# Optimization experiments

Measured on AMD Instinct MI355X. Metric: run time of the kernel, lower is better.

Reference implementation:

```python
import jax, jax.numpy as jnp
import numpy as np

B, C, H, W = 2, 64, 256, 256
CQ = C // 8    # query/key channels
CR = C // 16   # ShareChannelAttention reduction


def _conv1x1(x, w, b):
    # x: [B,C,H,W], w: [O,C], b: [O]  (1x1 conv == per-pixel linear)
    return jnp.einsum('bchw,oc->bohw', x, w) + b[None, :, None, None]


def _criss_cross(q, k, v):
    # q,k: [B,CQ,H,W], v: [B,C,H,W]; row+column attention with -inf on the
    # H-diagonal, softmax over concatenated H+W energies.
    Hh = q.shape[2]
    eH = jnp.einsum('bchw,bcgw->bhwg', q, k)                 # column (over h') energies
    eH = jnp.where(jnp.eye(Hh, dtype=bool)[:, None, :], -jnp.inf, eH)
    eW = jnp.einsum('bchw,bchv->bhwv', q, k)                 # row (over w') energies
    att = jax.nn.softmax(jnp.concatenate([eH, eW], axis=-1), axis=-1)  # [B,H,W,H+W]
    aH, aW = att[..., :Hh], att[..., Hh:]
    outH = jnp.einsum('bhwg,bcgw->bchw', aH, v)
    outW = jnp.einsum('bhwv,bchv->bchw', aW, v)
    return outH + outW


def _shareca(xa, xb, w1, b1, w2, b2):
    s = xa + xb
    def mlp(p):
        return _conv1x1(jax.nn.relu(_conv1x1(p, w1, b1)), w2, b2)
    gate = jax.nn.sigmoid(mlp(s.mean(axis=(2, 3), keepdims=True)) +
                          mlp(s.max(axis=(2, 3), keepdims=True)))
    return gate * s  # gate*xa + gate*xb


def _bn_relu(x, scale, bias):
    # BatchNorm2d in training mode (batch statistics, biased variance), eps=1e-5
    m = x.mean(axis=(0, 2, 3), keepdims=True)
    v = x.var(axis=(0, 2, 3), keepdims=True)
    xn = (x - m) * jax.lax.rsqrt(v + 1e-5)
    return jax.nn.relu(xn * scale[None, :, None, None] + bias[None, :, None, None])


def setup_inputs() -> dict:
    key = jax.random.key(0)
    ks = jax.random.split(key, 32)
    def n(k, shape, s=0.05):
        return jax.random.normal(k, shape, dtype=jnp.float32) * s
    inp = {
        'x1': n(ks[0], (B, C, H, W), 1.0),
        'x2': n(ks[1], (B, C, H, W), 1.0),
        'wq1': n(ks[2], (CQ, C)), 'bq1': n(ks[3], (CQ,)),
        'wq2': n(ks[4], (CQ, C)), 'bq2': n(ks[5], (CQ,)),
        'wk1': n(ks[6], (CQ, C)), 'bk1': n(ks[7], (CQ,)),
        'wk2': n(ks[8], (CQ, C)), 'bk2': n(ks[9], (CQ,)),
        'wv1': n(ks[10], (C, C)), 'bv1': n(ks[11], (C,)),
        'wv2': n(ks[12], (C, C)), 'bv2': n(ks[13], (C,)),
        'gamma1': n(ks[14], (1,), 0.5), 'gamma2': n(ks[15], (1,), 0.5),
        'sc1_w1': n(ks[16], (CR, C)), 'sc1_b1': n(ks[17], (CR,)),
        'sc1_w2': n(ks[18], (C, CR)), 'sc1_b2': n(ks[19], (C,)),
        'sc2_w1': n(ks[20], (CR, C)), 'sc2_b1': n(ks[21], (CR,)),
        'sc2_w2': n(ks[22], (C, CR)), 'sc2_b2': n(ks[23], (C,)),
        'bn1_scale': jnp.ones((C,), jnp.float32), 'bn1_bias': n(ks[24], (C,)),
        'bn2_scale': jnp.ones((C,), jnp.float32), 'bn2_bias': n(ks[25], (C,)),
    }
    return inp


def reference(x1, x2, wq1, bq1, wq2, bq2, wk1, bk1, wk2, bk2,
              wv1, bv1, wv2, bv2, gamma1, gamma2,
              sc1_w1, sc1_b1, sc1_w2, sc1_b2,
              sc2_w1, sc2_b1, sc2_w2, sc2_b2,
              bn1_scale, bn1_bias, bn2_scale, bn2_bias):
    q1 = _conv1x1(x1, wq1, bq1); q2 = _conv1x1(x2, wq2, bq2)
    k1 = _conv1x1(x1, wk1, bk1); k2 = _conv1x1(x2, wk2, bk2)
    v1 = _conv1x1(x1, wv1, bv1); v2 = _conv1x1(x2, wv2, bv2)
    att1 = _criss_cross(q2, k1, v1)  # out_H_1 + out_W_1
    att2 = _criss_cross(q1, k2, v2)  # out_H_2 + out_W_2
    x_1 = _shareca(gamma2 * att2 + x2, x1, sc1_w1, sc1_b1, sc1_w2, sc1_b2)
    x_2 = _shareca(gamma1 * att1 + x1, x2, sc2_w1, sc2_b1, sc2_w2, sc2_b2)
    out1 = _bn_relu(x_1 + x1, bn1_scale, bn1_bias)
    out2 = _bn_relu(x_2 + x2, bn2_scale, bn2_bias)
    # channel exchange: even channels keep the original input
    mask = (jnp.arange(C) % 2 == 0)[None, :, None, None]
    return jnp.where(mask, x1, out1), jnp.where(mask, x2, out2)
```

## Files before the change

kernel.cpp:

```cpp
#include <hip/hip_runtime.h>
#include <hip/hip_bf16.h>
#include <cstdint>
#include <cstddef>

typedef unsigned short bf16t;
typedef __attribute__((ext_vector_type(8))) short bf16x8;
typedef __attribute__((ext_vector_type(4))) float f32x4;

__device__ __forceinline__ unsigned short f2bf(float f) {
    unsigned u = __float_as_uint(f);
    u += 0x7fffu + ((u >> 16) & 1u);
    return (unsigned short)(u >> 16);
}
__device__ __forceinline__ float bf2f(unsigned short h) {
    return __uint_as_float(((unsigned)h) << 16);
}
__device__ __forceinline__ float bflo(unsigned u) { return __uint_as_float(u << 16); }
__device__ __forceinline__ float bfhi(unsigned u) { return __uint_as_float(u & 0xffff0000u); }
__device__ __forceinline__ unsigned pk2(float a, float b) {
    __hip_bfloat162 h = __float22bfloat162_rn(make_float2(a, b));
    return *(unsigned*)&h;
}
__device__ __forceinline__ bf16x8 mk8(unsigned a, unsigned b, unsigned c, unsigned d) {
    union { uint4 u; bf16x8 v; } cv; cv.u = make_uint4(a, b, c, d); return cv.v;
}

__device__ __forceinline__ unsigned fenc(float f) {
    unsigned u = __float_as_uint(f);
    return (u & 0x80000000u) ? ~u : (u | 0x80000000u);
}
__device__ __forceinline__ float fdec(unsigned u) {
    return __uint_as_float((u & 0x80000000u) ? (u ^ 0x80000000u) : ~u);
}

#define HW 65536

struct ConvArgs {
    const float* x[2];
    const float* wq[2]; const float* bq[2];
    const float* wk[2]; const float* bk[2];
    const float* wv[2]; const float* bv[2];
    bf16t* q[2]; bf16t* k[2]; bf16t* v[2];
    unsigned* zeroR;
};

__global__ __launch_bounds__(256) void conv_qkv(ConvArgs A)
{
    __shared__ __align__(16) bf16t Xlds[256 * 68];

    const int t = threadIdx.x;
    const int z = blockIdx.z;
    const int s = z >> 1, b = z & 1;
    if (z == 0 && blockIdx.x == 0) {
#pragma unroll
        for (int i = 0; i < 6; i++) A.zeroR[t + i * 256] = 0u;
    }
    const int lane = t & 63, wv = t >> 6, quad = lane >> 4, l16 = lane & 15;
    const int px0 = blockIdx.x * 256;

    const float* xp = A.x[s] + (size_t)b * 64 * HW + px0 + t;
    {
        unsigned xw[32];
#pragma unroll
        for (int c = 0; c < 32; c++)
            xw[c] = pk2(xp[(size_t)(2 * c) * HW], xp[(size_t)(2 * c + 1) * HW]);
#pragma unroll
        for (int g = 0; g < 16; g++)
            *(uint2*)&Xlds[t * 68 + g * 4] = make_uint2(xw[2 * g], xw[2 * g + 1]);
    }

    bf16x8 bfr[5][2];
    float bo[5];
    bf16t* obase[5];
#pragma unroll
    for (int ot = 0; ot < 5; ot++) {
        const int o = ot * 16 + l16;
        const float* wrow;
        if (o < 8)       { wrow = A.wq[s] + o * 64;        bo[ot] = A.bq[s][o];
                           obase[ot] = A.q[s] + (size_t)(b * 8 + o) * HW; }
        else if (o < 16) { wrow = A.wk[s] + (o - 8) * 64;  bo[ot] = A.bk[s][o - 8];
                           obase[ot] = A.k[s] + (size_t)(b * 8 + o - 8) * HW; }
        else             { wrow = A.wv[s] + (o - 16) * 64; bo[ot] = A.bv[s][o - 16];
                           obase[ot] = A.v[s] + (size_t)(b * 64 + o - 16) * HW; }
#pragma unroll
        for (int ks = 0; ks < 2; ks++) {
            const float* wp = wrow + ks * 32 + quad * 8;
            bfr[ot][ks] = mk8(pk2(wp[0], wp[1]), pk2(wp[2], wp[3]),
                              pk2(wp[4], wp[5]), pk2(wp[6], wp[7]));
        }
    }

    __syncthreads();

    bf16x8 afr[4][2];
#pragma unroll
    for (int i = 0; i < 4; i++)
#pragma unroll
        for (int ks = 0; ks < 2; ks++) {
            const int base = (wv * 64 + i * 16 + l16) * 68 + ks * 32 + quad * 8;
            const uint2 lo = *(const uint2*)&Xlds[base];
            const uint2 hi = *(const uint2*)&Xlds[base + 4];
            afr[i][ks] = mk8(lo.x, lo.y, hi.x, hi.y);
        }

    const f32x4 z4 = {0.f, 0.f, 0.f, 0.f};
    f32x4 acc[4][5];
#pragma unroll
    for (int i = 0; i < 4; i++)
#pragma unroll
        for (int ot = 0; ot < 5; ot++) acc[i][ot] = z4;

#pragma unroll
    for (int ks = 0; ks < 2; ks++)
#pragma unroll
        for (int i = 0; i < 4; i++)
#pragma unroll
            for (int ot = 0; ot < 5; ot++)
                acc[i][ot] = __builtin_amdgcn_mfma_f32_16x16x32_bf16(afr[i][ks], bfr[ot][ks], acc[i][ot], 0, 0, 0);

#pragma unroll
    for (int i = 0; i < 4; i++) {
        const int px = px0 + wv * 64 + i * 16 + quad * 4;
#pragma unroll
        for (int ot = 0; ot < 5; ot++) {
            uint2 u;
            u.x = pk2(acc[i][ot][0] + bo[ot], acc[i][ot][1] + bo[ot]);
            u.y = pk2(acc[i][ot][2] + bo[ot], acc[i][ot][3] + bo[ot]);
            *(uint2*)&obase[ot][px] = u;
        }
    }
}

__global__ __launch_bounds__(256) void transpose16(const bf16t* __restrict__ in, bf16t* __restrict__ out)
{
    __shared__ bf16t tile[64][68];
    const size_t zo = (size_t)blockIdx.z * HW;
    const int i0 = blockIdx.y * 64, j0 = blockIdx.x * 64;
    const int lc = threadIdx.x & 63, rg = threadIdx.x >> 6;
#pragma unroll
    for (int rr = 0; rr < 16; rr++) {
        int row = rg * 16 + rr;
        tile[row][lc] = in[zo + (size_t)(i0 + row) * 256 + j0 + lc];
    }
    __syncthreads();
#pragma unroll
    for (int rr = 0; rr < 16; rr++) {
        int row = rg * 16 + rr;
        out[zo + (size_t)(j0 + row) * 256 + i0 + lc] = tile[lc][row];
    }
}

struct RowccArgs {
    const bf16t* q[4]; const bf16t* k[4]; const bf16t* v[4];
    bf16t* o[4]; float* so[4];
};

__global__ __launch_bounds__(256, 3) void rowcc_mfma(RowccArgs P)
{
    __shared__ __align__(16) bf16t vs[64 * 264];

    const int t = threadIdx.x;
    const int r = blockIdx.x, b = blockIdx.y, z = blockIdx.z;
    const bool mask = (z < 2);
    const int lane = t & 63, wv = t >> 6, quad = lane >> 4, l16 = lane & 15;
    const int wband = wv * 64;
    const int jperm = 8 * (l16 >> 2) + (l16 & 3);

    const bf16t* qp = P.q[z];
    const bf16t* kp = P.k[z];
    const bf16t* vp = P.v[z];

    const size_t vb = (size_t)b * 64 * HW + (size_t)r * 256;
#pragma unroll
    for (int i = 0; i < 8; i++) {
        const int qd = i * 256 + t;
        const int c = qd >> 5, jc = (qd & 31) * 8;
        *(uint4*)&vs[c * 264 + jc] = *(const uint4*)&vp[vb + (size_t)c * HW + jc];
    }

    const bf16x8 zfr = {0, 0, 0, 0, 0, 0, 0, 0};
    bf16x8 qfr[4] = {zfr, zfr, zfr, zfr};
    const size_t rowb = (size_t)b * 8 * HW + (size_t)r * 256;
    if (quad == 0) {
#pragma unroll
        for (int wt = 0; wt < 4; wt++) {
            const int w_g = wband + wt * 16 + l16;
#pragma unroll
            for (int ch = 0; ch < 8; ch++)
                qfr[wt][ch] = (short)qp[rowb + (size_t)ch * HW + w_g];
        }
    }

    const f32x4 z4 = {0.f, 0.f, 0.f, 0.f};
    f32x4 acc[4][4];
#pragma unroll
    for (int i = 0; i < 4; i++)
#pragma unroll
        for (int j = 0; j < 4; j++) acc[i][j] = z4;
    float s_t[4] = {0.f, 0.f, 0.f, 0.f};

    bf16x8 kcur[2] = {zfr, zfr};
    if (quad == 0) {
#pragma unroll
        for (int jtile = 0; jtile < 2; jtile++)
#pragma unroll
            for (int ch = 0; ch < 8; ch++)
                kcur[jtile][ch] = (short)kp[rowb + (size_t)ch * HW + jtile * 4 + jperm];
    }

    __syncthreads();

    for (int jt = 0; jt < 8; jt++) {
        const int j0 = jt * 32;

        bf16x8 bfr[4];
#pragma unroll
        for (int ct = 0; ct < 4; ct++)
            bfr[ct] = *(const bf16x8*)&vs[(ct * 16 + l16) * 264 + j0 + quad * 8];

        bf16x8 knext[2] = {zfr, zfr};
        if (jt < 7 && quad == 0) {
            const int jn = (jt + 1) * 32;
#pragma unroll
            for (int jtile = 0; jtile < 2; jtile++)
#pragma unroll
                for (int ch = 0; ch < 8; ch++)
                    knext[jtile][ch] = (short)kp[rowb + (size_t)ch * HW + jn + jtile * 4 + jperm];
        }

        const bool dodiag = mask && ((jt >> 1) == wv);

#pragma unroll
        for (int wt = 0; wt < 4; wt++) {
            f32x4 e0 = __builtin_amdgcn_mfma_f32_16x16x32_bf16(kcur[0], qfr[wt], z4, 0, 0, 0);
            f32x4 e1 = __builtin_amdgcn_mfma_f32_16x16x32_bf16(kcur[1], qfr[wt], z4, 0, 0, 0);

            if (dodiag) {
                const int w_g = wband + wt * 16 + l16;
                const int jb = j0 + 8 * quad;
#pragma unroll
                for (int rr = 0; rr < 4; rr++) {
                    if (jb + rr == w_g)     e0[rr] = -3.0e38f;
                    if (jb + 4 + rr == w_g) e1[rr] = -3.0e38f;
                }
            }

            float p[8];
#pragma unroll
            for (int rr = 0; rr < 4; rr++) {
                p[rr]     = __expf(e0[rr]);
                p[4 + rr] = __expf(e1[rr]);
            }
            s_t[wt] += ((p[0] + p[1]) + (p[2] + p[3])) + ((p[4] + p[5]) + (p[6] + p[7]));
            const bf16x8 pa = mk8(pk2(p[0], p[1]), pk2(p[2], p[3]),
                                  pk2(p[4], p[5]), pk2(p[6], p[7]));

#pragma unroll
            for (int ct = 0; ct < 4; ct++)
                acc[wt][ct] = __builtin_amdgcn_mfma_f32_16x16x32_bf16(pa, bfr[ct], acc[wt][ct], 0, 0, 0);
        }

        kcur[0] = knext[0]; kcur[1] = knext[1];
    }

#pragma unroll
    for (int wt = 0; wt < 4; wt++) {
        float s = s_t[wt];
        s += __shfl_xor(s, 16, 64);
        s += __shfl_xor(s, 32, 64);
        s_t[wt] = s;
    }
    if (quad == 0) {
#pragma unroll
        for (int wt = 0; wt < 4; wt++) {
            const int w_g = wband + wt * 16 + l16;
            if (mask)
                P.so[z][(size_t)b * HW + w_g * 256 + r] = s_t[wt];
            else
                P.so[z][(size_t)b * HW + r * 256 + w_g] = s_t[wt];
        }
    }

    __syncthreads();
    bf16t* o_lds = vs;
#pragma unroll
    for (int wt = 0; wt < 4; wt++) {
        const int w0 = wband + wt * 16 + quad * 4;
#pragma unroll
        for (int ct = 0; ct < 4; ct++) {
            const int c = ct * 16 + l16;
            uint2 u;
            u.x = pk2(acc[wt][ct][0], acc[wt][ct][1]);
            u.y = pk2(acc[wt][ct][2], acc[wt][ct][3]);
            *(uint2*)&o_lds[c * 264 + w0] = u;
        }
    }
    __syncthreads();
    bf16t* ob = P.o[z] + (size_t)b * 64 * HW + (size_t)r * 256;
#pragma unroll
    for (int i = 0; i < 8; i++) {
        const int qd = i * 256 + t;
        const int c = qd >> 5, w8 = (qd & 31) * 8;
        *(uint4*)&ob[(size_t)c * HW + w8] = *(const uint4*)&o_lds[c * 264 + w8];
    }
}

__global__ __launch_bounds__(256) void combine_reduce(
    const bf16t* __restrict__ oH1, const bf16t* __restrict__ oW1,
    const bf16t* __restrict__ oH2, const bf16t* __restrict__ oW2,
    const float* __restrict__ sH1, const float* __restrict__ sW1,
    const float* __restrict__ sH2, const float* __restrict__ sW2,
    const float* __restrict__ x1, const float* __restrict__ x2,
    const float* __restrict__ gamma1, const float* __restrict__ gamma2,
    bf16t* __restrict__ s1, bf16t* __restrict__ s2,
    float* __restrict__ accum, unsigned* __restrict__ accmax)
{
    const int t = threadIdx.x, chunk = blockIdx.x, c = blockIdx.y, b = blockIdx.z;
    const float g1v = gamma1[0], g2v = gamma2[0];
    const size_t cb = ((size_t)(b * 64 + c)) * HW;
    const size_t pb = (size_t)b * HW;
    const bool codd = (c & 1) != 0;

    float pS1 = 0, pSS1 = 0, pSX1 = 0, pX1 = 0, pXX1 = 0, pM1 = -3e38f;
    float pS2 = 0, pSS2 = 0, pSX2 = 0, pX2 = 0, pXX2 = 0, pM2 = -3e38f;

    for (int i = 0; i < 16; i++) {
        const int pidx = chunk * 4096 + i * 256 + t;
        const float inv1 = 1.f / (sH1[pb + pidx] + sW1[pb + pidx]);
        const float inv2 = 1.f / (sH2[pb + pidx] + sW2[pb + pidx]);
        const float a1 = (bf2f(oH1[cb + pidx]) + bf2f(oW1[cb + pidx])) * inv1;
        const float a2 = (bf2f(oH2[cb + pidx]) + bf2f(oW2[cb + pidx])) * inv2;
        const float x1v = x1[cb + pidx], x2v = x2[cb + pidx];
        const float s1v = g2v * a2 + x2v + x1v;
        const float s2v = g1v * a1 + x1v + x2v;
        if (codd) {
            s1[cb + pidx] = f2bf(s1v);
            s2[cb + pidx] = f2bf(s2v);
        }
        pS1 += s1v; pSS1 += s1v * s1v; pSX1 += s1v * x1v; pX1 += x1v; pXX1 += x1v * x1v; pM1 = fmaxf(pM1, s1v);
        pS2 += s2v; pSS2 += s2v * s2v; pSX2 += s2v * x2v; pX2 += x2v; pXX2 += x2v * x2v; pM2 = fmaxf(pM2, s2v);
    }

    __shared__ float wred[12][4];
    float vals[12] = {pS1, pSS1, pSX1, pX1, pXX1, pM1, pS2, pSS2, pSX2, pX2, pXX2, pM2};
    const int lane = t & 63, wave = t >> 6;
#pragma unroll
    for (int iv = 0; iv < 12; iv++) {
        float v = vals[iv];
        const bool isMax = (iv == 5 || iv == 11);
#pragma unroll
        for (int off = 32; off > 0; off >>= 1) {
            const float o = __shfl_down(v, off, 64);
            v = isMax ? fmaxf(v, o) : (v + o);
        }
        if (lane == 0) wred[iv][wave] = v;
    }
    __syncthreads();
    if (t < 12) {
        const bool isMax = (t == 5 || t == 11);
        float v = wred[t][0];
        for (int i = 1; i < 4; i++) v = isMax ? fmaxf(v, wred[t][i]) : (v + wred[t][i]);
        const int stream = (t >= 6) ? 1 : 0;
        const int kk = t - stream * 6;
        if (kk == 5) atomicMax(&accmax[(stream * 2 + b) * 64 + c], fenc(v));
        else atomicAdd(&accum[((stream * 2 + b) * 64 + c) * 5 + kk], v);
    }
}

__global__ __launch_bounds__(256) void gates_bn(
    const float* __restrict__ accum, const unsigned* __restrict__ accmax,
    const float* __restrict__ sc1_w1, const float* __restrict__ sc1_b1,
    const float* __restrict__ sc1_w2, const float* __restrict__ sc1_b2,
    const float* __restrict__ sc2_w1, const float* __restrict__ sc2_b1,
    const float* __restrict__ sc2_w2, const float* __restrict__ sc2_b2,
    const float* __restrict__ bn1_scale, const float* __restrict__ bn1_bias,
    const float* __restrict__ bn2_scale, const float* __restrict__ bn2_bias,
    float* __restrict__ gates, float* __restrict__ AB)
{
    const int t = threadIdx.x;
    const int stream = t >> 7, b = (t >> 6) & 1, c = t & 63;
    __shared__ float meanS[256], maxS[256], e1S[256], e2S[256];

    const float S = accum[t * 5 + 0], SS = accum[t * 5 + 1], SX = accum[t * 5 + 2];
    const float X = accum[t * 5 + 3], XX = accum[t * 5 + 4];
    meanS[t] = S * (1.f / 65536.f);
    maxS[t] = fdec(accmax[t]);
    __syncthreads();

    const float* w1 = stream ? sc2_w1 : sc1_w1;
    const float* b1 = stream ? sc2_b1 : sc1_b1;
    const float* w2 = stream ? sc2_w2 : sc1_w2;
    const float* b2 = stream ? sc2_b2 : sc1_b2;
    float om = b2[c], ox = b2[c];
    const int base = stream * 128 + b * 64;
#pragma unroll
    for (int r = 0; r < 4; r++) {
        float hm = b1[r], hx = b1[r];
        for (int cc = 0; cc < 64; cc++) {
            hm += w1[r * 64 + cc] * meanS[base + cc];
            hx += w1[r * 64 + cc] * maxS[base + cc];
        }
        hm = fmaxf(hm, 0.f); hx = fmaxf(hx, 0.f);
        om += w2[c * 4 + r] * hm;
        ox += w2[c * 4 + r] * hx;
    }
    const float gate = 1.f / (1.f + __expf(-(om + ox)));
    gates[t] = gate;
    e1S[t] = gate * S + X;
    e2S[t] = gate * gate * SS + 2.f * gate * SX + XX;
    __syncthreads();
    if (b == 0) {
        const float sumY = e1S[t] + e1S[t + 64];
        const float sumY2 = e2S[t] + e2S[t + 64];
        const float meanY = sumY * (1.f / 131072.f);
        const float varY = sumY2 * (1.f / 131072.f) - meanY * meanY;
        const float sc = stream ? bn2_scale[c] : bn1_scale[c];
        const float bi = stream ? bn2_bias[c] : bn1_bias[c];
        const float A = sc * rsqrtf(varY + 1e-5f);
        AB[stream * 128 + c] = A;
        AB[stream * 128 + 64 + c] = bi - meanY * A;
    }
}

__global__ __launch_bounds__(256) void finalize(
    const bf16t* __restrict__ s1, const bf16t* __restrict__ s2,
    const float* __restrict__ x1, const float* __restrict__ x2,
    const float* __restrict__ gates, const float* __restrict__ AB,
    float* __restrict__ out)
{
    const size_t tid = (size_t)blockIdx.x * 256 + threadIdx.x;
    const size_t idx = tid * 4;
    const int b = (int)(idx >> 22);
    const int c = (int)((idx >> 16) & 63);
    const bool odd = (c & 1) != 0;

    const float4 x1v = *(const float4*)(x1 + idx);
    const float4 x2v = *(const float4*)(x2 + idx);
    float xa[4] = {x1v.x, x1v.y, x1v.z, x1v.w};
    float xb[4] = {x2v.x, x2v.y, x2v.z, x2v.w};
    float o1[4], o2[4];

    if (odd) {
        const float g1 = gates[b * 64 + c], g2 = gates[128 + b * 64 + c];
        const float A1 = AB[c], B1 = AB[64 + c], A2 = AB[128 + c], B2 = AB[192 + c];
        const uint2 su1 = *(const uint2*)(s1 + idx);
        const uint2 su2 = *(const uint2*)(s2 + idx);
        float s1f[4] = {bflo(su1.x), bfhi(su1.x), bflo(su1.y), bfhi(su1.y)};
        float s2f[4] = {bflo(su2.x), bfhi(su2.x), bflo(su2.y), bfhi(su2.y)};
#pragma unroll
        for (int j = 0; j < 4; j++) {
            const float y1 = g1 * s1f[j] + xa[j];
            const float y2 = g2 * s2f[j] + xb[j];
            o1[j] = fmaxf(A1 * y1 + B1, 0.f);
            o2[j] = fmaxf(A2 * y2 + B2, 0.f);
        }
    } else {
#pragma unroll
        for (int j = 0; j < 4; j++) { o1[j] = xa[j]; o2[j] = xb[j]; }
    }
    *(float4*)(out + idx) = make_float4(o1[0], o1[1], o1[2], o1[3]);
    *(float4*)(out + 8388608 + idx) = make_float4(o2[0], o2[1], o2[2], o2[3]);
}

extern "C" void kernel_launch(void* const* d_in, const int* in_sizes, int n_in,
                              void* d_out, int out_size, void* d_ws, size_t ws_size,
                              hipStream_t stream) {
    (void)in_sizes; (void)n_in; (void)out_size; (void)ws_size;
    const float* x1 = (const float*)d_in[0];
    const float* x2 = (const float*)d_in[1];
    const float* wq1 = (const float*)d_in[2];  const float* bq1 = (const float*)d_in[3];
    const float* wq2 = (const float*)d_in[4];  const float* bq2 = (const float*)d_in[5];
    const float* wk1 = (const float*)d_in[6];  const float* bk1 = (const float*)d_in[7];
    const float* wk2 = (const float*)d_in[8];  const float* bk2 = (const float*)d_in[9];
    const float* wv1 = (const float*)d_in[10]; const float* bv1 = (const float*)d_in[11];
    const float* wv2 = (const float*)d_in[12]; const float* bv2 = (const float*)d_in[13];
    const float* gamma1 = (const float*)d_in[14];
    const float* gamma2 = (const float*)d_in[15];
    const float* sc1_w1 = (const float*)d_in[16]; const float* sc1_b1 = (const float*)d_in[17];
    const float* sc1_w2 = (const float*)d_in[18]; const float* sc1_b2 = (const float*)d_in[19];
    const float* sc2_w1 = (const float*)d_in[20]; const float* sc2_b1 = (const float*)d_in[21];
    const float* sc2_w2 = (const float*)d_in[22]; const float* sc2_b2 = (const float*)d_in[23];
    const float* bn1_scale = (const float*)d_in[24]; const float* bn1_bias = (const float*)d_in[25];
    const float* bn2_scale = (const float*)d_in[26]; const float* bn2_bias = (const float*)d_in[27];

    char* p = (char*)d_ws;
    const size_t SZ_QK = 2097152;
    const size_t SZ_V = 16777216;
    const size_t SZ_ST = 524288;

    bf16t* q1 = (bf16t*)(p + 0 * SZ_QK);
    bf16t* k1 = (bf16t*)(p + 1 * SZ_QK);
    bf16t* q2 = (bf16t*)(p + 2 * SZ_QK);
    bf16t* k2 = (bf16t*)(p + 3 * SZ_QK);
    bf16t* v1 = (bf16t*)(p + 4 * SZ_QK);
    bf16t* v2 = (bf16t*)(p + 4 * SZ_QK + SZ_V);
    size_t off = 4 * SZ_QK + 2 * SZ_V;
    bf16t* q1T = (bf16t*)(p + off + 0 * SZ_QK);
    bf16t* k1T = (bf16t*)(p + off + 1 * SZ_QK);
    bf16t* q2T = (bf16t*)(p + off + 2 * SZ_QK);
    bf16t* k2T = (bf16t*)(p + off + 3 * SZ_QK);
    bf16t* v1T = (bf16t*)(p + off + 4 * SZ_QK);
    bf16t* v2T = (bf16t*)(p + off + 4 * SZ_QK + SZ_V);
    off += 4 * SZ_QK + 2 * SZ_V;
    bf16t* oH1T = (bf16t*)(p + off); off += SZ_V;
    bf16t* oH2T = (bf16t*)(p + off); off += SZ_V;
    bf16t* oW1 = (bf16t*)(p + off); off += SZ_V;
    bf16t* oW2 = (bf16t*)(p + off); off += SZ_V;
    float* sH1 = (float*)(p + off); off += SZ_ST;
    float* sH2 = (float*)(p + off); off += SZ_ST;
    float* sW1 = (float*)(p + off); off += SZ_ST;
    float* sW2 = (float*)(p + off); off += SZ_ST;
    float* accum = (float*)(p + off);
    unsigned* accmax = (unsigned*)(p + off + 5120);
    float* gates = (float*)(p + off + 6144);
    float* AB = (float*)(p + off + 7168);

    bf16t* oH1 = v1T;
    bf16t* oH2 = v2T;
    bf16t* s1 = oH1T;
    bf16t* s2 = oH2T;

    ConvArgs CA;
    CA.x[0] = x1; CA.x[1] = x2;
    CA.wq[0] = wq1; CA.wq[1] = wq2; CA.bq[0] = bq1; CA.bq[1] = bq2;
    CA.wk[0] = wk1; CA.wk[1] = wk2; CA.bk[0] = bk1; CA.bk[1] = bk2;
    CA.wv[0] = wv1; CA.wv[1] = wv2; CA.bv[0] = bv1; CA.bv[1] = bv2;
    CA.q[0] = q1; CA.q[1] = q2; CA.k[0] = k1; CA.k[1] = k2;
    CA.v[0] = v1; CA.v[1] = v2;
    CA.zeroR = (unsigned*)accum;
    conv_qkv<<<dim3(256, 1, 4), 256, 0, stream>>>(CA);

    transpose16<<<dim3(4, 4, 320), 256, 0, stream>>>(q1, q1T);

    RowccArgs RA;
    RA.q[0] = q2T; RA.k[0] = k1T; RA.v[0] = v1T; RA.o[0] = oH1T; RA.so[0] = sH1;
    RA.q[1] = q1T; RA.k[1] = k2T; RA.v[1] = v2T; RA.o[1] = oH2T; RA.so[1] = sH2;
    RA.q[2] = q2;  RA.k[2] = k1;  RA.v[2] = v1;  RA.o[2] = oW1;  RA.so[2] = sW1;
    RA.q[3] = q1;  RA.k[3] = k2;  RA.v[3] = v2;  RA.o[3] = oW2;  RA.so[3] = sW2;
    rowcc_mfma<<<dim3(256, 2, 4), 256, 0, stream>>>(RA);

    transpose16<<<dim3(4, 4, 256), 256, 0, stream>>>(oH1T, oH1);

    combine_reduce<<<dim3(16, 64, 2), 256, 0, stream>>>(
        oH1, oW1, oH2, oW2, sH1, sW1, sH2, sW2, x1, x2, gamma1, gamma2,
        s1, s2, accum, accmax);

    gates_bn<<<1, 256, 0, stream>>>(accum, accmax,
                                    sc1_w1, sc1_b1, sc1_w2, sc1_b2,
                                    sc2_w1, sc2_b1, sc2_w2, sc2_b2,
                                    bn1_scale, bn1_bias, bn2_scale, bn2_bias,
                                    gates, AB);

    finalize<<<8192, 256, 0, stream>>>(s1, s2, x1, x2, gates, AB, (float*)d_out);
}
```

Before: 309.8 us.

## Fuse oH transpose into combine_reduce, write even channels early, vectorize transpose

```diff
diff --git a/kernel.cpp b/kernel.cpp
--- a/kernel.cpp
+++ b/kernel.cpp
@@ -133,20 +133,27 @@
 
 __global__ __launch_bounds__(256) void transpose16(const bf16t* __restrict__ in, bf16t* __restrict__ out)
 {
-    __shared__ bf16t tile[64][68];
+    __shared__ unsigned tile[64][33];
     const size_t zo = (size_t)blockIdx.z * HW;
     const int i0 = blockIdx.y * 64, j0 = blockIdx.x * 64;
-    const int lc = threadIdx.x & 63, rg = threadIdx.x >> 6;
-#pragma unroll
-    for (int rr = 0; rr < 16; rr++) {
-        int row = rg * 16 + rr;
-        tile[row][lc] = in[zo + (size_t)(i0 + row) * 256 + j0 + lc];
-    }
-    __syncthreads();
-#pragma unroll
-    for (int rr = 0; rr < 16; rr++) {
-        int row = rg * 16 + rr;
-        out[zo + (size_t)(j0 + row) * 256 + i0 + lc] = tile[lc][row];
+    const int cp = threadIdx.x & 31;
+    const int r8 = threadIdx.x >> 5;
+#pragma unroll
+    for (int rr = 0; rr < 8; rr++) {
+        const int row = rr * 8 + r8;
+        tile[row][cp] = *(const unsigned*)&in[zo + (size_t)(i0 + row) * 256 + j0 + cp * 2];
+    }
+    __syncthreads();
+    const int ip = threadIdx.x & 31;
+    const int j8 = threadIdx.x >> 5;
+#pragma unroll
+    for (int jj = 0; jj < 8; jj++) {
+        const int j = jj * 8 + j8;
+        const unsigned a = tile[2 * ip][j >> 1];
+        const unsigned b = tile[2 * ip + 1][j >> 1];
+        const unsigned lo = (j & 1) ? (a >> 16) : (a & 0xffffu);
+        const unsigned hi = (j & 1) ? (b >> 16) : (b & 0xffffu);
+        *(unsigned*)&out[zo + (size_t)(j0 + j) * 256 + i0 + ip * 2] = lo | (hi << 16);
     }
 }
 
@@ -306,39 +313,71 @@
 }
 
 __global__ __launch_bounds__(256) void combine_reduce(
-    const bf16t* __restrict__ oH1, const bf16t* __restrict__ oW1,
-    const bf16t* __restrict__ oH2, const bf16t* __restrict__ oW2,
+    const bf16t* __restrict__ oH1T, const bf16t* __restrict__ oW1,
+    const bf16t* __restrict__ oH2T, const bf16t* __restrict__ oW2,
     const float* __restrict__ sH1, const float* __restrict__ sW1,
     const float* __restrict__ sH2, const float* __restrict__ sW2,
     const float* __restrict__ x1, const float* __restrict__ x2,
     const float* __restrict__ gamma1, const float* __restrict__ gamma2,
     bf16t* __restrict__ s1, bf16t* __restrict__ s2,
+    float* __restrict__ out1, float* __restrict__ out2,
     float* __restrict__ accum, unsigned* __restrict__ accmax)
 {
-    const int t = threadIdx.x, chunk = blockIdx.x, c = blockIdx.y, b = blockIdx.z;
+    __shared__ bf16t oth1[64][66];
+    __shared__ bf16t oth2[64][66];
+
+    const int t = threadIdx.x, wblk = blockIdx.x, c = blockIdx.y, b = blockIdx.z;
     const float g1v = gamma1[0], g2v = gamma2[0];
     const size_t cb = ((size_t)(b * 64 + c)) * HW;
     const size_t pb = (size_t)b * HW;
     const bool codd = (c & 1) != 0;
+    const int w0 = wblk * 64;
+    const int w = w0 + (t & 63);
+    const int wv = t >> 6;
+    const int hq = t & 15, wl = t >> 4;
 
     float pS1 = 0, pSS1 = 0, pSX1 = 0, pX1 = 0, pXX1 = 0, pM1 = -3e38f;
     float pS2 = 0, pSS2 = 0, pSX2 = 0, pX2 = 0, pXX2 = 0, pM2 = -3e38f;
 
-    for (int i = 0; i < 16; i++) {
-        const int pidx = chunk * 4096 + i * 256 + t;
-        const float inv1 = 1.f / (sH1[pb + pidx] + sW1[pb + pidx]);
-        const float inv2 = 1.f / (sH2[pb + pidx] + sW2[pb + pidx]);
-        const float a1 = (bf2f(oH1[cb + pidx]) + bf2f(oW1[cb + pidx])) * inv1;
-        const float a2 = (bf2f(oH2[cb + pidx]) + bf2f(oW2[cb + pidx])) * inv2;
-        const float x1v = x1[cb + pidx], x2v = x2[cb + pidx];
-        const float s1v = g2v * a2 + x2v + x1v;
-        const float s2v = g1v * a1 + x1v + x2v;
-        if (codd) {
-            s1[cb + pidx] = f2bf(s1v);
-            s2[cb + pidx] = f2bf(s2v);
-        }
-        pS1 += s1v; pSS1 += s1v * s1v; pSX1 += s1v * x1v; pX1 += x1v; pXX1 += x1v * x1v; pM1 = fmaxf(pM1, s1v);
-        pS2 += s2v; pSS2 += s2v * s2v; pSX2 += s2v * x2v; pX2 += x2v; pXX2 += x2v * x2v; pM2 = fmaxf(pM2, s2v);
+    for (int hb = 0; hb < 4; hb++) {
+        __syncthreads();
+#pragma unroll
+        for (int p = 0; p < 4; p++) {
+            const int wll = wl + p * 16;
+            const size_t g = cb + (size_t)(w0 + wll) * 256 + hb * 64 + hq * 4;
+            const uint2 u1 = *(const uint2*)&oH1T[g];
+            const uint2 u2 = *(const uint2*)&oH2T[g];
+            const int hl = hq * 4;
+            oth1[hl + 0][wll] = (bf16t)(u1.x & 0xffffu);
+            oth1[hl + 1][wll] = (bf16t)(u1.x >> 16);
+            oth1[hl + 2][wll] = (bf16t)(u1.y & 0xffffu);
+            oth1[hl + 3][wll] = (bf16t)(u1.y >> 16);
+            oth2[hl + 0][wll] = (bf16t)(u2.x & 0xffffu);
+            oth2[hl + 1][wll] = (bf16t)(u2.x >> 16);
+            oth2[hl + 2][wll] = (bf16t)(u2.y & 0xffffu);
+            oth2[hl + 3][wll] = (bf16t)(u2.y >> 16);
+        }
+        __syncthreads();
+        for (int hh = 0; hh < 16; hh++) {
+            const int hl = wv * 16 + hh;
+            const int pidx = (hb * 64 + hl) * 256 + w;
+            const float inv1 = 1.f / (sH1[pb + pidx] + sW1[pb + pidx]);
+            const float inv2 = 1.f / (sH2[pb + pidx] + sW2[pb + pidx]);
+            const float a1 = (bf2f(oth1[hl][w - w0]) + bf2f(oW1[cb + pidx])) * inv1;
+            const float a2 = (bf2f(oth2[hl][w - w0]) + bf2f(oW2[cb + pidx])) * inv2;
+            const float x1v = x1[cb + pidx], x2v = x2[cb + pidx];
+            const float s1v = g2v * a2 + x2v + x1v;
+            const float s2v = g1v * a1 + x1v + x2v;
+            if (codd) {
+                s1[cb + pidx] = f2bf(s1v);
+                s2[cb + pidx] = f2bf(s2v);
+            } else {
+                out1[cb + pidx] = x1v;
+                out2[cb + pidx] = x2v;
+            }
+            pS1 += s1v; pSS1 += s1v * s1v; pSX1 += s1v * x1v; pX1 += x1v; pXX1 += x1v * x1v; pM1 = fmaxf(pM1, s1v);
+            pS2 += s2v; pSS2 += s2v * s2v; pSX2 += s2v * x2v; pX2 += x2v; pXX2 += x2v * x2v; pM2 = fmaxf(pM2, s2v);
+        }
     }
 
     __shared__ float wred[12][4];
@@ -429,34 +468,30 @@
     float* __restrict__ out)
 {
     const size_t tid = (size_t)blockIdx.x * 256 + threadIdx.x;
-    const size_t idx = tid * 4;
-    const int b = (int)(idx >> 22);
-    const int c = (int)((idx >> 16) & 63);
-    const bool odd = (c & 1) != 0;
-
+    const size_t u = tid * 4;
+    const int b = (int)(u >> 21);
+    const int c = 2 * (int)((u >> 16) & 31) + 1;
+    const size_t px = u & 65535u;
+    const size_t idx = ((size_t)b << 22) + ((size_t)c << 16) + px;
+
+    const float g1 = gates[b * 64 + c], g2 = gates[128 + b * 64 + c];
+    const float A1 = AB[c], B1 = AB[64 + c], A2 = AB[128 + c], B2 = AB[192 + c];
+
+    const uint2 su1 = *(const uint2*)(s1 + idx);
+    const uint2 su2 = *(const uint2*)(s2 + idx);
     const float4 x1v = *(const float4*)(x1 + idx);
     const float4 x2v = *(const float4*)(x2 + idx);
+    float s1f[4] = {bflo(su1.x), bfhi(su1.x), bflo(su1.y), bfhi(su1.y)};
+    float s2f[4] = {bflo(su2.x), bfhi(su2.x), bflo(su2.y), bfhi(su2.y)};
     float xa[4] = {x1v.x, x1v.y, x1v.z, x1v.w};
     float xb[4] = {x2v.x, x2v.y, x2v.z, x2v.w};
     float o1[4], o2[4];
-
-    if (odd) {
-        const float g1 = gates[b * 64 + c], g2 = gates[128 + b * 64 + c];
-        const float A1 = AB[c], B1 = AB[64 + c], A2 = AB[128 + c], B2 = AB[192 + c];
-        const uint2 su1 = *(const uint2*)(s1 + idx);
-        const uint2 su2 = *(const uint2*)(s2 + idx);
-        float s1f[4] = {bflo(su1.x), bfhi(su1.x), bflo(su1.y), bfhi(su1.y)};
-        float s2f[4] = {bflo(su2.x), bfhi(su2.x), bflo(su2.y), bfhi(su2.y)};
-#pragma unroll
-        for (int j = 0; j < 4; j++) {
-            const float y1 = g1 * s1f[j] + xa[j];
-            const float y2 = g2 * s2f[j] + xb[j];
-            o1[j] = fmaxf(A1 * y1 + B1, 0.f);
-            o2[j] = fmaxf(A2 * y2 + B2, 0.f);
-        }
-    } else {
-#pragma unroll
-        for (int j = 0; j < 4; j++) { o1[j] = xa[j]; o2[j] = xb[j]; }
+#pragma unroll
+    for (int j = 0; j < 4; j++) {
+        const float y1 = g1 * s1f[j] + xa[j];
+        const float y2 = g2 * s2f[j] + xb[j];
+        o1[j] = fmaxf(A1 * y1 + B1, 0.f);
+        o2[j] = fmaxf(A2 * y2 + B2, 0.f);
     }
     *(float4*)(out + idx) = make_float4(o1[0], o1[1], o1[2], o1[3]);
     *(float4*)(out + 8388608 + idx) = make_float4(o2[0], o2[1], o2[2], o2[3]);
@@ -515,10 +550,8 @@
     float* gates = (float*)(p + off + 6144);
     float* AB = (float*)(p + off + 7168);
 
-    bf16t* oH1 = v1T;
-    bf16t* oH2 = v2T;
-    bf16t* s1 = oH1T;
-    bf16t* s2 = oH2T;
+    bf16t* s1 = v1T;
+    bf16t* s2 = v2T;
 
     ConvArgs CA;
     CA.x[0] = x1; CA.x[1] = x2;
@@ -539,11 +572,9 @@
     RA.q[3] = q1;  RA.k[3] = k2;  RA.v[3] = v2;  RA.o[3] = oW2;  RA.so[3] = sW2;
     rowcc_mfma<<<dim3(256, 2, 4), 256, 0, stream>>>(RA);
 
-    transpose16<<<dim3(4, 4, 256), 256, 0, stream>>>(oH1T, oH1);
-
-    combine_reduce<<<dim3(16, 64, 2), 256, 0, stream>>>(
-        oH1, oW1, oH2, oW2, sH1, sW1, sH2, sW2, x1, x2, gamma1, gamma2,
-        s1, s2, accum, accmax);
+    combine_reduce<<<dim3(4, 64, 2), 256, 0, stream>>>(
+        oH1T, oW1, oH2T, oW2, sH1, sW1, sH2, sW2, x1, x2, gamma1, gamma2,
+        s1, s2, (float*)d_out, (float*)d_out + 8388608, accum, accmax);
 
     gates_bn<<<1, 256, 0, stream>>>(accum, accmax,
                                     sc1_w1, sc1_b1, sc1_w2, sc1_b2,
@@ -551,5 +582,5 @@
                                     bn1_scale, bn1_bias, bn2_scale, bn2_bias,
                                     gates, AB);
 
-    finalize<<<8192, 256, 0, stream>>>(s1, s2, x1, x2, gates, AB, (float*)d_out);
-}
+    finalize<<<4096, 256, 0, stream>>>(s1, s2, x1, x2, gates, AB, (float*)d_out);
+}
```

New measurement: 319.9 us. 1.03x slower.
